# Optimization experiments

Measured on AMD Instinct MI355X. Metric: run time of the kernel, lower is better.

## Reference

```python
import jax, jax.numpy as jnp
import numpy as np

D_MODEL = 1024
NUM_HEADS = 16
D_K = D_MODEL // NUM_HEADS


def setup_inputs() -> dict:
    key = jax.random.key(0)
    kq, kk, kv, k1, k2, k3, k4 = jax.random.split(key, 7)
    B, S = 2, 2048
    # Xavier-uniform init for square [d_model, d_model] weights
    limit = float(np.sqrt(6.0 / (D_MODEL + D_MODEL)))
    def xav(k):
        return jax.random.uniform(k, (D_MODEL, D_MODEL), jnp.float32, -limit, limit)
    return {
        "query": jax.random.normal(kq, (B, S, D_MODEL), jnp.float32),
        "key": jax.random.normal(kk, (B, S, D_MODEL), jnp.float32),
        "value": jax.random.normal(kv, (B, S, D_MODEL), jnp.float32),
        "W_q": xav(k1),
        "W_k": xav(k2),
        "W_v": xav(k3),
        "W_o": xav(k4),
    }


def reference(query, key, value, W_q, W_k, W_v, W_o):
    B, Sq, _ = query.shape
    Sk = key.shape[1]
    # Linear layers: y = x @ W.T (torch nn.Linear convention)
    Q = (query @ W_q.T).reshape(B, Sq, NUM_HEADS, D_K).transpose(0, 2, 1, 3)
    K = (key @ W_k.T).reshape(B, Sk, NUM_HEADS, D_K).transpose(0, 2, 1, 3)
    V = (value @ W_v.T).reshape(B, Sk, NUM_HEADS, D_K).transpose(0, 2, 1, 3)
    scale = 1.0 / jnp.sqrt(jnp.asarray(D_K, Q.dtype))
    scores = jnp.einsum("bhqd,bhkd->bhqk", Q, K) * scale  # [B,H,Sq,Sk]
    attn = jax.nn.softmax(scores, axis=-1)
    # dropout is identity in eval mode
    out = jnp.einsum("bhqk,bhkd->bhqd", attn, V)
    out = out.transpose(0, 2, 1, 3).reshape(B, Sq, D_MODEL)
    return out @ W_o.T
```

## Files before the change

### kernel.cpp

```cpp
#include <hip/hip_runtime.h>
#include <math.h>

typedef unsigned short ushort_t;
typedef __attribute__((ext_vector_type(8))) short short8;
typedef __attribute__((ext_vector_type(4))) float f32x4;
typedef __attribute__((ext_vector_type(16))) float f32x16;
typedef __attribute__((ext_vector_type(4))) unsigned short ushort4v;
typedef __attribute__((ext_vector_type(2))) unsigned int uint2v;
typedef __attribute__((ext_vector_type(4))) unsigned int uint4v;

#define D_MODEL 1024
#define SEQ 2048
#define MROWS 4096
#define PLANE (MROWS * D_MODEL)
#define WELEM (D_MODEL * D_MODEL)

static __device__ __forceinline__ ushort_t f2bf(float f) {
    unsigned u = __builtin_bit_cast(unsigned, f);
    return (ushort_t)((u + 0x7fffu + ((u >> 16) & 1u)) >> 16);
}
static __device__ __forceinline__ unsigned cvtpk(float lo, float hi) {
    unsigned r;
    asm("v_cvt_pk_bf16_f32 %0, %1, %2" : "=v"(r) : "v"(lo), "v"(hi));
    return r;
}

#define GLDS16(gp, lp)                                                         \
    __builtin_amdgcn_global_load_lds(                                          \
        (const __attribute__((address_space(1))) void*)(gp),                   \
        (__attribute__((address_space(3))) void*)(lp), 16, 0, 0)

__global__ __launch_bounds__(256)
void cvt_all(const float* __restrict__ q, const float* __restrict__ k,
             const float* __restrict__ v, const float* __restrict__ w0,
             const float* __restrict__ w1, const float* __restrict__ w2,
             const float* __restrict__ w3, ushort_t* __restrict__ dst) {
    int blk = blockIdx.x;
    const float* s;
    size_t base;
    if (blk < 6144) {
        const int p = blk >> 11;
        s = (p == 0) ? q : (p == 1) ? k : v;
        base = (size_t)p * PLANE;
        blk &= 2047;
    } else {
        const int p = (blk - 6144) >> 9;
        s = (p == 0) ? w0 : (p == 1) ? w1 : (p == 2) ? w2 : w3;
        base = 3 * (size_t)PLANE + (size_t)p * WELEM;
        blk = (blk - 6144) & 511;
    }
    const int i = (blk * 256 + threadIdx.x) * 8;
    float4 a = *(const float4*)(s + i);
    float4 bb = *(const float4*)(s + i + 4);
    short8 o;
    o[0] = (short)f2bf(a.x); o[1] = (short)f2bf(a.y);
    o[2] = (short)f2bf(a.z); o[3] = (short)f2bf(a.w);
    o[4] = (short)f2bf(bb.x); o[5] = (short)f2bf(bb.y);
    o[6] = (short)f2bf(bb.z); o[7] = (short)f2bf(bb.w);
    *(short8*)(dst + base + i) = o;
}

__global__ __launch_bounds__(256)
void gemm3(const ushort_t* __restrict__ Xq, const ushort_t* __restrict__ Wb,
           ushort_t* __restrict__ Cb) {
    __shared__ __align__(16) ushort_t As[128 * 64];
    __shared__ __align__(16) ushort_t Bs[128 * 64];

    const int z = blockIdx.z;
    const ushort_t* A = Xq + (size_t)z * PLANE;
    const ushort_t* B = Wb + (size_t)z * WELEM;
    ushort_t* C = Cb + (size_t)z * PLANE;

    const int tid = threadIdx.x;
    const int lane = tid & 63;
    const int wid = tid >> 6;
    const int wr = wid >> 1, wc = wid & 1;
    const int brow = blockIdx.y * 128;
    const int bcol = blockIdx.x * 128;

    const int lrow = lane >> 3;
    const int loff = ((lane & 7) ^ lrow) * 8;

    const ushort_t* aS[4];
    const ushort_t* bS[4];
#pragma unroll
    for (int i = 0; i < 4; ++i) {
        aS[i] = A + (size_t)(brow + wid * 32 + i * 8 + lrow) * D_MODEL + loff;
        bS[i] = B + (size_t)(bcol + wid * 32 + i * 8 + lrow) * D_MODEL + loff;
    }

    f32x4 acc[4][4];
#pragma unroll
    for (int i = 0; i < 4; ++i)
#pragma unroll
        for (int j = 0; j < 4; ++j) acc[i][j] = {0.f, 0.f, 0.f, 0.f};

    const int fr = lane & 15, fg = lane >> 4;

    for (int k0 = 0; k0 < D_MODEL; k0 += 64) {
        __syncthreads();
#pragma unroll
        for (int i = 0; i < 4; ++i) {
            GLDS16(aS[i] + k0, As + (wid * 32 + i * 8) * 64);
            GLDS16(bS[i] + k0, Bs + (wid * 32 + i * 8) * 64);
        }
        __syncthreads();
#pragma unroll
        for (int ks = 0; ks < 2; ++ks) {
            const int coff = (ks * 32 + fg * 8) ^ ((fr & 7) << 3);
            short8 af[4], bw[4];
#pragma unroll
            for (int mi = 0; mi < 4; ++mi)
                af[mi] = *(const short8*)&As[(wr * 64 + mi * 16 + fr) * 64 + coff];
#pragma unroll
            for (int nj = 0; nj < 4; ++nj)
                bw[nj] = *(const short8*)&Bs[(wc * 64 + nj * 16 + fr) * 64 + coff];
#pragma unroll
            for (int mi = 0; mi < 4; ++mi)
#pragma unroll
                for (int nj = 0; nj < 4; ++nj)
                    acc[mi][nj] = __builtin_amdgcn_mfma_f32_16x16x32_bf16(
                        af[mi], bw[nj], acc[mi][nj], 0, 0, 0);
        }
    }

    if (z < 2) {
#pragma unroll
        for (int mi = 0; mi < 4; ++mi)
#pragma unroll
            for (int nj = 0; nj < 4; ++nj) {
                const int n = bcol + wc * 64 + nj * 16 + fr;
#pragma unroll
                for (int r = 0; r < 4; ++r) {
                    const int m = brow + wr * 64 + mi * 16 + fg * 4 + r;
                    C[(size_t)m * D_MODEL + n] = f2bf(acc[mi][nj][r]);
                }
            }
    } else {
#pragma unroll
        for (int mi = 0; mi < 4; ++mi)
#pragma unroll
            for (int nj = 0; nj < 4; ++nj) {
                const int n = bcol + wc * 64 + nj * 16 + fr;
                const int m0 = brow + wr * 64 + mi * 16 + fg * 4;
                ushort4v o4;
#pragma unroll
                for (int r = 0; r < 4; ++r) o4[r] = f2bf(acc[mi][nj][r]);
                *(ushort4v*)&C[((size_t)(m0 >> 11) << 21) + (size_t)n * SEQ + (m0 & 2047)] = o4;
            }
    }
}

__global__ __launch_bounds__(256)
void gemm_wo(const ushort_t* __restrict__ A, const ushort_t* __restrict__ B,
             float* __restrict__ C) {
    __shared__ __align__(16) ushort_t As[128 * 64];
    __shared__ __align__(16) ushort_t Bs[128 * 64];

    const int tid = threadIdx.x;
    const int lane = tid & 63;
    const int wid = tid >> 6;
    const int wr = wid >> 1, wc = wid & 1;
    const int brow = blockIdx.y * 128;
    const int bcol = blockIdx.x * 128;

    const int lrow = lane >> 3;
    const int loff = ((lane & 7) ^ lrow) * 8;

    const ushort_t* aS[4];
    const ushort_t* bS[4];
#pragma unroll
    for (int i = 0; i < 4; ++i) {
        aS[i] = A + (size_t)(brow + wid * 32 + i * 8 + lrow) * D_MODEL + loff;
        bS[i] = B + (size_t)(bcol + wid * 32 + i * 8 + lrow) * D_MODEL + loff;
    }

    f32x4 acc[4][4];
#pragma unroll
    for (int i = 0; i < 4; ++i)
#pragma unroll
        for (int j = 0; j < 4; ++j) acc[i][j] = {0.f, 0.f, 0.f, 0.f};

    const int fr = lane & 15, fg = lane >> 4;

    for (int k0 = 0; k0 < D_MODEL; k0 += 64) {
        __syncthreads();
#pragma unroll
        for (int i = 0; i < 4; ++i) {
            GLDS16(aS[i] + k0, As + (wid * 32 + i * 8) * 64);
            GLDS16(bS[i] + k0, Bs + (wid * 32 + i * 8) * 64);
        }
        __syncthreads();
#pragma unroll
        for (int ks = 0; ks < 2; ++ks) {
            const int coff = (ks * 32 + fg * 8) ^ ((fr & 7) << 3);
            short8 af[4], bw[4];
#pragma unroll
            for (int mi = 0; mi < 4; ++mi)
                af[mi] = *(const short8*)&As[(wr * 64 + mi * 16 + fr) * 64 + coff];
#pragma unroll
            for (int nj = 0; nj < 4; ++nj)
                bw[nj] = *(const short8*)&Bs[(wc * 64 + nj * 16 + fr) * 64 + coff];
#pragma unroll
            for (int mi = 0; mi < 4; ++mi)
#pragma unroll
                for (int nj = 0; nj < 4; ++nj)
                    acc[mi][nj] = __builtin_amdgcn_mfma_f32_16x16x32_bf16(
                        af[mi], bw[nj], acc[mi][nj], 0, 0, 0);
        }
    }

#pragma unroll
    for (int mi = 0; mi < 4; ++mi)
#pragma unroll
        for (int nj = 0; nj < 4; ++nj) {
            const int n = bcol + wc * 64 + nj * 16 + fr;
#pragma unroll
            for (int r = 0; r < 4; ++r) {
                const int m = brow + wr * 64 + mi * 16 + fg * 4 + r;
                C[(size_t)m * D_MODEL + n] = acc[mi][nj][r];
            }
        }
}

__global__ __launch_bounds__(256)
void attn_mfma(const ushort_t* __restrict__ Qp, const ushort_t* __restrict__ Kp,
               const ushort_t* __restrict__ VT, ushort_t* __restrict__ Ap) {
    __shared__ __align__(16) ushort_t Ks[2][64 * 64];
    __shared__ __align__(16) ushort_t Vs[2][64 * 64];
    __shared__ __align__(16) ushort_t Qs[128 * 64];

    const int tid = threadIdx.x;
    const int lane = tid & 63;
    const int wid = tid >> 6;
    const int bid = blockIdx.x;
    const int qt = bid & 15;
    const int h = (bid >> 4) & 15;
    const int b = bid >> 8;

    const int lrow = lane >> 3;
    const int loff = ((lane & 7) ^ lrow) * 8;
    const int q31 = lane & 31;
    const int hi = lane >> 5;

    const int m0 = b * SEQ + qt * 128;

#pragma unroll
    for (int j = 0; j < 4; ++j) {
        const ushort_t* qS =
            Qp + (size_t)(m0 + wid * 32 + j * 8 + lrow) * D_MODEL + h * 64 + loff;
        GLDS16(qS, Qs + (wid * 32 + j * 8) * 64);
    }
    const ushort_t* kS[2];
    const ushort_t* vS[2];
#pragma unroll
    for (int j = 0; j < 2; ++j) {
        const int cr = wid * 16 + j * 8 + lrow;
        kS[j] = Kp + (size_t)(b * SEQ + cr) * D_MODEL + h * 64 + loff;
        vS[j] = VT + ((size_t)b << 21) + (size_t)(h * 64 + cr) * SEQ + loff;
        GLDS16(kS[j], Ks[0] + (wid * 16 + j * 8) * 64);
        GLDS16(vS[j], Vs[0] + (wid * 16 + j * 8) * 64);
        kS[j] += 64 * D_MODEL;
        vS[j] += 64;
    }
    __syncthreads();

    const int qrow = wid * 32 + q31;
    const int rsw = (q31 & 7);
    short8 aq[4];
#pragma unroll
    for (int s = 0; s < 4; ++s)
        aq[s] = *(const short8*)&Qs[qrow * 64 + (((s * 2 + hi) ^ rsw) * 8)];

    f32x16 accO[2];
#pragma unroll
    for (int db = 0; db < 2; ++db)
#pragma unroll
        for (int r = 0; r < 16; ++r) accO[db][r] = 0.f;
    float m_s = -INFINITY;
    float l_p = 0.f;

    const float CEXP = 0.18033688011112042f;

    int cur = 0;
    for (int kt = 0; kt < SEQ / 64; ++kt) {
        __syncthreads();
        if (kt + 1 < SEQ / 64) {
#pragma unroll
            for (int j = 0; j < 2; ++j) {
                GLDS16(kS[j], Ks[cur ^ 1] + (wid * 16 + j * 8) * 64);
                GLDS16(vS[j], Vs[cur ^ 1] + (wid * 16 + j * 8) * 64);
                kS[j] += 64 * D_MODEL;
                vS[j] += 64;
            }
        }

        f32x16 accS[2];
#pragma unroll
        for (int kb = 0; kb < 2; ++kb)
#pragma unroll
            for (int r = 0; r < 16; ++r) accS[kb][r] = 0.f;
        __builtin_amdgcn_s_setprio(1);
#pragma unroll
        for (int s = 0; s < 4; ++s)
#pragma unroll
            for (int kb = 0; kb < 2; ++kb) {
                short8 ak = *(const short8*)&Ks[cur][(kb * 32 + q31) * 64 +
                                                     (((s * 2 + hi) ^ rsw) * 8)];
                accS[kb] = __builtin_amdgcn_mfma_f32_32x32x16_bf16(
                    ak, aq[s], accS[kb], 0, 0, 0);
            }
        __builtin_amdgcn_s_setprio(0);

        float mx = accS[0][0];
#pragma unroll
        for (int kb = 0; kb < 2; ++kb)
#pragma unroll
            for (int r = 0; r < 16; ++r) mx = fmaxf(mx, accS[kb][r]);
        mx = fmaxf(mx, __shfl_xor(mx, 32));
        const float cand = mx * CEXP;
        if (__any(cand > m_s + 8.f)) {
            const float mnew = fmaxf(m_s, cand);
            const float al = __builtin_amdgcn_exp2f(m_s - mnew);
            m_s = mnew;
            l_p *= al;
#pragma unroll
            for (int db = 0; db < 2; ++db)
#pragma unroll
                for (int r = 0; r < 16; ++r) accO[db][r] *= al;
        }
        float ps = 0.f;
        const float nm = -m_s;
#pragma unroll
        for (int kb = 0; kb < 2; ++kb)
#pragma unroll
            for (int r = 0; r < 16; ++r) {
                const float p = __builtin_amdgcn_exp2f(fmaf(accS[kb][r], CEXP, nm));
                accS[kb][r] = p;
                ps += p;
            }
        l_p += ps;

        short8 pf[4];
#pragma unroll
        for (int ks4 = 0; ks4 < 4; ++ks4) {
            const int kb = ks4 >> 1;
            const int bse = (ks4 & 1) * 8;
            unsigned w0 = cvtpk(accS[kb][bse + 0], accS[kb][bse + 1]);
            unsigned w1 = cvtpk(accS[kb][bse + 2], accS[kb][bse + 3]);
            unsigned w2 = cvtpk(accS[kb][bse + 4], accS[kb][bse + 5]);
            unsigned w3 = cvtpk(accS[kb][bse + 6], accS[kb][bse + 7]);
            asm("v_permlane32_swap_b32 %0, %1" : "+v"(w0), "+v"(w2));
            asm("v_permlane32_swap_b32 %0, %1" : "+v"(w1), "+v"(w3));
            uint4v u = {w0, w1, w2, w3};
            pf[ks4] = __builtin_bit_cast(short8, u);
        }

        __builtin_amdgcn_s_setprio(1);
#pragma unroll
        for (int db = 0; db < 2; ++db)
#pragma unroll
            for (int ks4 = 0; ks4 < 4; ++ks4) {
                short8 av = *(const short8*)&Vs[cur][(db * 32 + q31) * 64 +
                                                     (((ks4 * 2 + hi) ^ rsw) * 8)];
                accO[db] = __builtin_amdgcn_mfma_f32_32x32x16_bf16(
                    av, pf[ks4], accO[db], 0, 0, 0);
            }
        __builtin_amdgcn_s_setprio(0);
        cur ^= 1;
    }

    float lt = l_p + __shfl_xor(l_p, 32);
    const float inv = 1.0f / lt;
    unsigned* QsW = (unsigned*)Qs;
    const int kkw = 2 * (q31 & 15);
#pragma unroll
    for (int db = 0; db < 2; ++db)
#pragma unroll
        for (int blk = 0; blk < 4; ++blk) {
            const int c0 = 4 * blk + 2 * hi + 16 * db;
            uint2v u;
            u[0] = cvtpk(accO[db][4 * blk + 0] * inv, accO[db][4 * blk + 1] * inv);
            u[1] = cvtpk(accO[db][4 * blk + 2] * inv, accO[db][4 * blk + 3] * inv);
            *(uint2v*)&QsW[qrow * 32 + (c0 ^ kkw)] = u;
        }
    __syncthreads();
#pragma unroll
    for (int pass = 0; pass < 4; ++pass) {
        const int r = wid * 32 + pass * 8 + (lane >> 3);
        const int g8 = lane & 7;
        const int kk = 2 * (r & 15);
        uint2v u0 = *(const uint2v*)&QsW[r * 32 + ((4 * g8) ^ kk)];
        uint2v u1 = *(const uint2v*)&QsW[r * 32 + ((4 * g8 + 2) ^ kk)];
        uint4v o = {u0[0], u0[1], u1[0], u1[1]};
        *(uint4v*)&Ap[(size_t)(m0 + r) * D_MODEL + h * 64 + g8 * 8] = o;
    }
}

extern "C" void kernel_launch(void* const* d_in, const int* in_sizes, int n_in,
                              void* d_out, int out_size, void* d_ws, size_t ws_size,
                              hipStream_t stream) {
    const float* query = (const float*)d_in[0];
    const float* key   = (const float*)d_in[1];
    const float* value = (const float*)d_in[2];
    const float* W_q   = (const float*)d_in[3];
    const float* W_k   = (const float*)d_in[4];
    const float* W_v   = (const float*)d_in[5];
    const float* W_o   = (const float*)d_in[6];
    float* out = (float*)d_out;

    ushort_t* ws = (ushort_t*)d_ws;
    ushort_t* Xq = ws;
    ushort_t* Wb = ws + 3 * (size_t)PLANE;
    ushort_t* Qp = ws + 4 * (size_t)PLANE;
    ushort_t* Kp = Qp + (size_t)PLANE;
    ushort_t* VT = Kp + (size_t)PLANE;
    ushort_t* Ap = VT + (size_t)PLANE;

    cvt_all<<<8192, 256, 0, stream>>>(query, key, value, W_q, W_k, W_v, W_o, Xq);

    dim3 g3(D_MODEL / 128, MROWS / 128, 3);
    gemm3<<<g3, 256, 0, stream>>>(Xq, Wb, Qp);

    attn_mfma<<<512, 256, 0, stream>>>(Qp, Kp, VT, Ap);

    dim3 go(D_MODEL / 128, MROWS / 128);
    gemm_wo<<<go, 256, 0, stream>>>(Ap, Wb + 3 * (size_t)WELEM, out);
}
```

Baseline: 140.5 us.

## Split attention KV tiles across two wave groups with merged softmax state

Doubles the attention block to 512 threads so that two groups of four waves each handle half of every 64-key tile for the same 32-query rows. Each wave keeps its own running max and sum. At the end the two partial outputs are merged through shared memory using rescaled weights. The aim is more waves per CU and shorter per-wave dependency chains between the QK MFMAs, the exp, and the PV MFMAs, which should help latency hiding on the 512-block grid. The cost is a cross-wave reduction epilogue, extra barriers, and a different per-wave running-max, which affects when the lazy rescaling fires.

```diff
diff --git a/kernel.cpp b/kernel.cpp
--- a/kernel.cpp
+++ b/kernel.cpp
@@ -223,16 +223,19 @@
         }
 }
 
-__global__ __launch_bounds__(256)
+__global__ __launch_bounds__(512, 4)
 void attn_mfma(const ushort_t* __restrict__ Qp, const ushort_t* __restrict__ Kp,
                const ushort_t* __restrict__ VT, ushort_t* __restrict__ Ap) {
-    __shared__ __align__(16) ushort_t Ks[2][64 * 64];
-    __shared__ __align__(16) ushort_t Vs[2][64 * 64];
+    __shared__ __align__(16) ushort_t KVbuf[2][2][4096];
     __shared__ __align__(16) ushort_t Qs[128 * 64];
+    __shared__ float sm[2][128];
+    __shared__ float sl[2][128];
 
     const int tid = threadIdx.x;
     const int lane = tid & 63;
     const int wid = tid >> 6;
+    const int qgrp = wid & 3;
+    const int khalf = wid >> 2;
     const int bid = blockIdx.x;
     const int qt = bid & 15;
     const int h = (bid >> 4) & 15;
@@ -246,27 +249,23 @@
     const int m0 = b * SEQ + qt * 128;
 
 #pragma unroll
-    for (int j = 0; j < 4; ++j) {
+    for (int j = 0; j < 2; ++j) {
         const ushort_t* qS =
-            Qp + (size_t)(m0 + wid * 32 + j * 8 + lrow) * D_MODEL + h * 64 + loff;
-        GLDS16(qS, Qs + (wid * 32 + j * 8) * 64);
-    }
-    const ushort_t* kS[2];
-    const ushort_t* vS[2];
-#pragma unroll
-    for (int j = 0; j < 2; ++j) {
-        const int cr = wid * 16 + j * 8 + lrow;
-        kS[j] = Kp + (size_t)(b * SEQ + cr) * D_MODEL + h * 64 + loff;
-        vS[j] = VT + ((size_t)b << 21) + (size_t)(h * 64 + cr) * SEQ + loff;
-        GLDS16(kS[j], Ks[0] + (wid * 16 + j * 8) * 64);
-        GLDS16(vS[j], Vs[0] + (wid * 16 + j * 8) * 64);
-        kS[j] += 64 * D_MODEL;
-        vS[j] += 64;
-    }
+            Qp + (size_t)(m0 + wid * 16 + j * 8 + lrow) * D_MODEL + h * 64 + loff;
+        GLDS16(qS, Qs + (wid * 16 + j * 8) * 64);
+    }
+    const ushort_t* kS =
+        Kp + (size_t)(b * SEQ + wid * 8 + lrow) * D_MODEL + h * 64 + loff;
+    const ushort_t* vS =
+        VT + ((size_t)b << 21) + (size_t)(h * 64 + wid * 8 + lrow) * SEQ + loff;
+    GLDS16(kS, KVbuf[0][0] + wid * 512);
+    GLDS16(vS, KVbuf[1][0] + wid * 512);
+    kS += 64 * D_MODEL;
+    vS += 64;
     __syncthreads();
 
-    const int qrow = wid * 32 + q31;
-    const int rsw = (q31 & 7);
+    const int qrow = qgrp * 32 + q31;
+    const int rsw = q31 & 7;
     short8 aq[4];
 #pragma unroll
     for (int s = 0; s < 4; ++s)
@@ -281,42 +280,33 @@
     float l_p = 0.f;
 
     const float CEXP = 0.18033688011112042f;
+    const int kbase = khalf * 32;
 
     int cur = 0;
     for (int kt = 0; kt < SEQ / 64; ++kt) {
         __syncthreads();
         if (kt + 1 < SEQ / 64) {
-#pragma unroll
-            for (int j = 0; j < 2; ++j) {
-                GLDS16(kS[j], Ks[cur ^ 1] + (wid * 16 + j * 8) * 64);
-                GLDS16(vS[j], Vs[cur ^ 1] + (wid * 16 + j * 8) * 64);
-                kS[j] += 64 * D_MODEL;
-                vS[j] += 64;
-            }
-        }
-
-        f32x16 accS[2];
-#pragma unroll
-        for (int kb = 0; kb < 2; ++kb)
-#pragma unroll
-            for (int r = 0; r < 16; ++r) accS[kb][r] = 0.f;
+            GLDS16(kS, KVbuf[0][cur ^ 1] + wid * 512);
+            GLDS16(vS, KVbuf[1][cur ^ 1] + wid * 512);
+            kS += 64 * D_MODEL;
+            vS += 64;
+        }
+
+        f32x16 accS;
+#pragma unroll
+        for (int r = 0; r < 16; ++r) accS[r] = 0.f;
         __builtin_amdgcn_s_setprio(1);
 #pragma unroll
-        for (int s = 0; s < 4; ++s)
-#pragma unroll
-            for (int kb = 0; kb < 2; ++kb) {
-                short8 ak = *(const short8*)&Ks[cur][(kb * 32 + q31) * 64 +
-                                                     (((s * 2 + hi) ^ rsw) * 8)];
-                accS[kb] = __builtin_amdgcn_mfma_f32_32x32x16_bf16(
-                    ak, aq[s], accS[kb], 0, 0, 0);
-            }
+        for (int s = 0; s < 4; ++s) {
+            short8 ak = *(const short8*)&KVbuf[0][cur][(kbase + q31) * 64 +
+                                                       (((s * 2 + hi) ^ rsw) * 8)];
+            accS = __builtin_amdgcn_mfma_f32_32x32x16_bf16(ak, aq[s], accS, 0, 0, 0);
+        }
         __builtin_amdgcn_s_setprio(0);
 
-        float mx = accS[0][0];
-#pragma unroll
-        for (int kb = 0; kb < 2; ++kb)
-#pragma unroll
-            for (int r = 0; r < 16; ++r) mx = fmaxf(mx, accS[kb][r]);
+        float mx = accS[0];
+#pragma unroll
+        for (int r = 1; r < 16; ++r) mx = fmaxf(mx, accS[r]);
         mx = fmaxf(mx, __shfl_xor(mx, 32));
         const float cand = mx * CEXP;
         if (__any(cand > m_s + 8.f)) {
@@ -332,62 +322,90 @@
         float ps = 0.f;
         const float nm = -m_s;
 #pragma unroll
-        for (int kb = 0; kb < 2; ++kb)
-#pragma unroll
-            for (int r = 0; r < 16; ++r) {
-                const float p = __builtin_amdgcn_exp2f(fmaf(accS[kb][r], CEXP, nm));
-                accS[kb][r] = p;
-                ps += p;
-            }
+        for (int r = 0; r < 16; ++r) {
+            const float p = __builtin_amdgcn_exp2f(fmaf(accS[r], CEXP, nm));
+            accS[r] = p;
+            ps += p;
+        }
         l_p += ps;
 
-        short8 pf[4];
-#pragma unroll
-        for (int ks4 = 0; ks4 < 4; ++ks4) {
-            const int kb = ks4 >> 1;
-            const int bse = (ks4 & 1) * 8;
-            unsigned w0 = cvtpk(accS[kb][bse + 0], accS[kb][bse + 1]);
-            unsigned w1 = cvtpk(accS[kb][bse + 2], accS[kb][bse + 3]);
-            unsigned w2 = cvtpk(accS[kb][bse + 4], accS[kb][bse + 5]);
-            unsigned w3 = cvtpk(accS[kb][bse + 6], accS[kb][bse + 7]);
+        short8 pf[2];
+#pragma unroll
+        for (int ks2 = 0; ks2 < 2; ++ks2) {
+            const int bse = ks2 * 8;
+            unsigned w0 = cvtpk(accS[bse + 0], accS[bse + 1]);
+            unsigned w1 = cvtpk(accS[bse + 2], accS[bse + 3]);
+            unsigned w2 = cvtpk(accS[bse + 4], accS[bse + 5]);
+            unsigned w3 = cvtpk(accS[bse + 6], accS[bse + 7]);
             asm("v_permlane32_swap_b32 %0, %1" : "+v"(w0), "+v"(w2));
             asm("v_permlane32_swap_b32 %0, %1" : "+v"(w1), "+v"(w3));
             uint4v u = {w0, w1, w2, w3};
-            pf[ks4] = __builtin_bit_cast(short8, u);
+            pf[ks2] = __builtin_bit_cast(short8, u);
         }
 
         __builtin_amdgcn_s_setprio(1);
 #pragma unroll
         for (int db = 0; db < 2; ++db)
 #pragma unroll
-            for (int ks4 = 0; ks4 < 4; ++ks4) {
-                short8 av = *(const short8*)&Vs[cur][(db * 32 + q31) * 64 +
-                                                     (((ks4 * 2 + hi) ^ rsw) * 8)];
+            for (int ks2 = 0; ks2 < 2; ++ks2) {
+                short8 av = *(const short8*)&KVbuf[1][cur][(db * 32 + q31) * 64 +
+                    (((khalf * 4 + ks2 * 2 + hi) ^ rsw) * 8)];
                 accO[db] = __builtin_amdgcn_mfma_f32_32x32x16_bf16(
-                    av, pf[ks4], accO[db], 0, 0, 0);
+                    av, pf[ks2], accO[db], 0, 0, 0);
             }
         __builtin_amdgcn_s_setprio(0);
         cur ^= 1;
     }
 
-    float lt = l_p + __shfl_xor(l_p, 32);
-    const float inv = 1.0f / lt;
+    const float lt = l_p + __shfl_xor(l_p, 32);
+    const int qg = qgrp * 32 + q31;
+    if (lane < 32) {
+        sm[khalf][qg] = m_s;
+        sl[khalf][qg] = lt;
+    }
+    __syncthreads();
+    const float mA = sm[0][qg], mB = sm[1][qg];
+    const float mC = fmaxf(mA, mB);
+    const float wA = __builtin_amdgcn_exp2f(mA - mC);
+    const float wB = __builtin_amdgcn_exp2f(mB - mC);
+    const float inv = 1.0f / (wA * sl[0][qg] + wB * sl[1][qg]);
+
+    float* O1 = (float*)KVbuf;
+    if (khalf == 1) {
+#pragma unroll
+        for (int db = 0; db < 2; ++db)
+#pragma unroll
+            for (int rq = 0; rq < 4; ++rq) {
+                f32x4 v;
+#pragma unroll
+                for (int j = 0; j < 4; ++j) v[j] = accO[db][rq * 4 + j] * wB;
+                const int c = db * 8 + rq * 2 + hi;
+                *(f32x4*)&O1[qg * 64 + ((c ^ (q31 & 15)) * 4)] = v;
+            }
+    }
+    __syncthreads();
     unsigned* QsW = (unsigned*)Qs;
-    const int kkw = 2 * (q31 & 15);
-#pragma unroll
-    for (int db = 0; db < 2; ++db)
-#pragma unroll
-        for (int blk = 0; blk < 4; ++blk) {
-            const int c0 = 4 * blk + 2 * hi + 16 * db;
-            uint2v u;
-            u[0] = cvtpk(accO[db][4 * blk + 0] * inv, accO[db][4 * blk + 1] * inv);
-            u[1] = cvtpk(accO[db][4 * blk + 2] * inv, accO[db][4 * blk + 3] * inv);
-            *(uint2v*)&QsW[qrow * 32 + (c0 ^ kkw)] = u;
-        }
+    if (khalf == 0) {
+        const int kkw = 2 * (q31 & 15);
+#pragma unroll
+        for (int db = 0; db < 2; ++db)
+#pragma unroll
+            for (int rq = 0; rq < 4; ++rq) {
+                const int c = db * 8 + rq * 2 + hi;
+                f32x4 o1 = *(const f32x4*)&O1[qg * 64 + ((c ^ (q31 & 15)) * 4)];
+                float o0 = (accO[db][rq * 4 + 0] * wA + o1[0]) * inv;
+                float o1v = (accO[db][rq * 4 + 1] * wA + o1[1]) * inv;
+                float o2 = (accO[db][rq * 4 + 2] * wA + o1[2]) * inv;
+                float o3 = (accO[db][rq * 4 + 3] * wA + o1[3]) * inv;
+                uint2v u = {cvtpk(o0, o1v), cvtpk(o2, o3)};
+                const int c0 = 4 * rq + 2 * hi + 16 * db;
+                *(uint2v*)&QsW[qrow * 32 + (c0 ^ kkw)] = u;
+            }
+    }
     __syncthreads();
 #pragma unroll
-    for (int pass = 0; pass < 4; ++pass) {
-        const int r = wid * 32 + pass * 8 + (lane >> 3);
+    for (int pass = 0; pass < 2; ++pass) {
+        const int r = wid * 16 + pass * 8 + (lane >> 3);
         const int g8 = lane & 7;
         const int kk = 2 * (r & 15);
         uint2v u0 = *(const uint2v*)&QsW[r * 32 + ((4 * g8) ^ kk)];
@@ -422,7 +440,7 @@
     dim3 g3(D_MODEL / 128, MROWS / 128, 3);
     gemm3<<<g3, 256, 0, stream>>>(Xq, Wb, Qp);
 
-    attn_mfma<<<512, 256, 0, stream>>>(Qp, Kp, VT, Ap);
+    attn_mfma<<<512, 512, 0, stream>>>(Qp, Kp, VT, Ap);
 
     dim3 go(D_MODEL / 128, MROWS / 128);
     gemm_wo<<<go, 256, 0, stream>>>(Ap, Wb + 3 * (size_t)WELEM, out);
```

Result: faster. 131.8 us (-6.2%).
